# Kernel optimization log

Measured on AMD Instinct MI355X. Metric: run time of the kernel, lower is better.

## Reference

```python
import jax, jax.numpy as jnp
import numpy as np
from jax import lax

EPS = 1e-5

def setup_inputs() -> dict:
    key = jax.random.key(0)
    k1, k2 = jax.random.split(key)
    x = jax.random.normal(k1, (8, 256, 64, 64), dtype=jnp.float32)
    W = jax.random.normal(k2, (128, 256, 5, 5), dtype=jnp.float32) * 0.02
    gamma = jnp.ones((128,), dtype=jnp.float32)
    beta = jnp.zeros((128,), dtype=jnp.float32)
    return {"x": x, "W": W, "gamma": gamma, "beta": beta}

def reference(x, W, gamma, beta):
    B, C, H, Wd = x.shape
    # bilinear x2 upsample, half-pixel centers (== torch align_corners=False)
    up = jax.image.resize(x, (B, C, 2 * H, 2 * Wd), method="bilinear")
    # conv2d, stride 1, padding 2, no bias (norm == 'BN')
    out = lax.conv_general_dilated(
        up, W, window_strides=(1, 1), padding=[(2, 2), (2, 2)],
        dimension_numbers=("NCHW", "OIHW", "NCHW"))
    # BatchNorm2d (batch statistics, training-style refresh)
    mean = jnp.mean(out, axis=(0, 2, 3))
    var = jnp.var(out, axis=(0, 2, 3))
    inv = gamma / jnp.sqrt(var + EPS)
    out = (out - mean[None, :, None, None]) * inv[None, :, None, None] + beta[None, :, None, None]
    # activation: torch.relu
    return jax.nn.relu(out)
```

## Files before the change

kernel.cpp:

```cpp
#include <hip/hip_runtime.h>
#include <hip/hip_bf16.h>
#include <stdint.h>

typedef short s8v __attribute__((ext_vector_type(8)));
typedef float f4v __attribute__((ext_vector_type(4)));

__device__ __forceinline__ void async_copy16(const void* gsrc, void* lds_dst) {
  __builtin_amdgcn_global_load_lds(
      (const __attribute__((address_space(1))) uint32_t*)(uintptr_t)gsrc,
      (__attribute__((address_space(3))) uint32_t*)(uint32_t)(uintptr_t)lds_dst,
      16, 0, 0);
}

#define WAITVM(N) asm volatile("s_waitcnt vmcnt(" #N ")" ::: "memory")
__device__ __forceinline__ void block_barrier() {
  asm volatile("" ::: "memory");
  __builtin_amdgcn_s_barrier();
  asm volatile("" ::: "memory");
}

__global__ __launch_bounds__(256) void wpack_kernel(const float* __restrict__ W,
                                                    __hip_bfloat16* __restrict__ Wr,
                                                    float* __restrict__ gstats) {
  __shared__ __hip_bfloat16 t[256 * 26];
  const int co = blockIdx.x;
  const int tid = threadIdx.x;
  if (co == 0) gstats[tid] = 0.f;
  const float* src = W + co * 6400;
  for (int i = tid; i < 6400; i += 256) {
    int ci = i / 25;
    int pos = i - ci * 25;
    t[ci * 26 + pos] = __float2bfloat16(src[i]);
  }
  __syncthreads();
  for (int pos = 0; pos < 25; ++pos)
    Wr[pos * 32768 + co * 256 + tid] = t[tid * 26 + pos];
}

__global__ __launch_bounds__(256, 2) void upsample_kernel(const float* __restrict__ x,
                                                          __hip_bfloat16* __restrict__ up) {
  __shared__ __hip_bfloat16 lx[10 * 48 * 66];
  const int tid = threadIdx.x;
  const int bx = blockIdx.x;
  const int owb = bx & 1;
  const int ohb = (bx >> 1) & 7;
  const int cb = (bx >> 4) & 3;
  const int b = bx >> 6;
  const int oh0 = ohb * 16, ow0 = owb * 64, c0 = cb * 64;
  const int ih0 = (oh0 >> 1) - 1;
  const int iw_lo = (ow0 >> 1) - 1;
  const int aligned = (iw_lo < 0 ? 0 : iw_lo) & ~15;

  for (int i = tid; i < 64 * 10 * 12; i += 256) {
    int c = i / 120;
    int rem = i - c * 120;
    int r = rem / 12;
    int w4 = (rem - r * 12) * 4;
    int gr = ih0 + r;
    gr = gr < 0 ? 0 : (gr > 63 ? 63 : gr);
    const float4 v = *(const float4*)&x[(((b * 256 + c0 + c) * 64) + gr) * 64 + aligned + w4];
    int base = (r * 48 + w4) * 66 + c;
    lx[base]       = __float2bfloat16(v.x);
    lx[base + 66]  = __float2bfloat16(v.y);
    lx[base + 132] = __float2bfloat16(v.z);
    lx[base + 198] = __float2bfloat16(v.w);
  }
  __syncthreads();

  const int c2 = (tid & 31) * 2;
  const int owq = tid >> 5;
  uint32_t* upu = (uint32_t*)up;
  for (int it = 0; it < 128; ++it) {
    int oh_l = it >> 3;
    int ow_l = (it & 7) * 8 + owq;
    int oh = oh0 + oh_l, ow = ow0 + ow_l;
    int ihA = (oh >> 1) - ((oh & 1) ^ 1);
    float wh = (oh & 1) ? 0.75f : 0.25f;
    int iwA = (ow >> 1) - ((ow & 1) ^ 1);
    float wwt = (ow & 1) ? 0.75f : 0.25f;
    int r0 = ihA - ih0;
    int w0 = (iwA < 0 ? 0 : iwA) - aligned;
    int w1t = iwA + 1; w1t = w1t > 63 ? 63 : w1t;
    int w1 = w1t - aligned;
    uint32_t t00 = *(const uint32_t*)&lx[(r0 * 48 + w0) * 66 + c2];
    uint32_t t01 = *(const uint32_t*)&lx[(r0 * 48 + w1) * 66 + c2];
    uint32_t t10 = *(const uint32_t*)&lx[((r0 + 1) * 48 + w0) * 66 + c2];
    uint32_t t11 = *(const uint32_t*)&lx[((r0 + 1) * 48 + w1) * 66 + c2];
    float wlo = wh * wwt, wlo1 = wh * (1.f - wwt);
    float whi = (1.f - wh) * wwt, whi1 = (1.f - wh) * (1.f - wwt);
    float vlo = wlo * __uint_as_float(t00 << 16) + wlo1 * __uint_as_float(t01 << 16) +
                whi * __uint_as_float(t10 << 16) + whi1 * __uint_as_float(t11 << 16);
    float vhi = wlo * __uint_as_float(t00 & 0xffff0000u) + wlo1 * __uint_as_float(t01 & 0xffff0000u) +
                whi * __uint_as_float(t10 & 0xffff0000u) + whi1 * __uint_as_float(t11 & 0xffff0000u);
    __hip_bfloat16 h0 = __float2bfloat16(vlo);
    __hip_bfloat16 h1 = __float2bfloat16(vhi);
    uint32_t pk = (uint32_t)(*(unsigned short*)&h0) | ((uint32_t)(*(unsigned short*)&h1) << 16);
    upu[((((size_t)(b * 128 + oh) * 128) + ow) * 256 + c0 + c2) >> 1] = pk;
  }
}

#define ASLOT 8448
__global__ __launch_bounds__(512, 2) void conv_kernel(const __hip_bfloat16* __restrict__ up,
                                                      const __hip_bfloat16* __restrict__ Wr,
                                                      float* __restrict__ out,
                                                      float* __restrict__ gstats) {
  __shared__ __align__(16) unsigned short lA[5 * ASLOT];
  __shared__ __align__(16) unsigned short lB[3][128 * 64];
  __shared__ float lsum[128], lssq[128];

  const int tid = threadIdx.x;
  const int lane = tid & 63;
  const int wave = tid >> 6;
  const int wm = wave >> 1;
  const int wn = wave & 1;
  const int lane15 = lane & 15;
  const int quad = lane >> 4;
  const int wb = wave << 6;

  const int bid = blockIdx.x;
  const int orig = ((bid & 7) << 5) | (bid >> 3);
  const int b = orig >> 5;
  const int oh0 = (orig & 31) << 2;

  const f4v zero4 = {0.f, 0.f, 0.f, 0.f};
  if (tid < 128) { lsum[tid] = 0.f; lssq[tid] = 0.f; }
  if (tid < 160) {
    int s = tid >> 5, j = tid & 31;
    int rsel = j >> 3;
    int r = (rsel < 2) ? rsel : (128 + rsel);
    *(f4v*)&lA[s * ASLOT + (r * 8 + (j & 7)) * 8] = zero4;
  }

  auto stageA = [&](int slot, const __hip_bfloat16* uprow) {
#pragma unroll
    for (int t = 0; t < 2; ++t) {
      int pl = t * 512 + wb + lane;
      int riw = pl >> 3, pc = pl & 7;
      int r = riw + 2;
      int cq = pc ^ (r & 7);
      async_copy16(uprow + riw * 256 + cq * 8, (void*)&lA[slot * ASLOT + (16 + t * 512 + wb) * 8]);
    }
  };
  auto stageB = [&](const __hip_bfloat16* wsrc, int bsel) {
#pragma unroll
    for (int t = 0; t < 2; ++t) {
      int pl = t * 512 + wb + lane;
      int n = pl >> 3, pc = pl & 7;
      int cq = pc ^ (n & 7);
      async_copy16(wsrc + n * 256 + cq * 8, (void*)&lB[bsel][(t * 512 + wb) * 8]);
    }
  };

  f4v acc[8][4];
#pragma unroll
  for (int i = 0; i < 8; ++i)
#pragma unroll
    for (int j = 0; j < 4; ++j) acc[i][j] = zero4;

  for (int rr = 0; rr < 4; ++rr) {
    int ih = oh0 + rr - 2;
    if ((unsigned)ih < 128u)
      stageA(ih % 5, up + (size_t)(b * 128 + ih) * 32768);
  }
  stageB(Wr, 0);
  __syncthreads();

  int bcur = 0;
  for (int cb = 0; cb < 4; ++cb) {
    const int c0 = cb << 6;
    for (int kh = 0; kh < 5; ++kh) {
      const int ih = oh0 + wm + kh - 2;
      const bool rowok = (unsigned)ih < 128u;
      const int abase = rowok ? (ih % 5) * ASLOT : 0;
      for (int kw = 0; kw < 5; ++kw) {
        const int pos = kh * 5 + kw;
        const int bnext = (bcur == 2) ? 0 : bcur + 1;
        if (cb != 0 && kh == 0 && kw == 0) {
          for (int rr = 0; rr < 4; ++rr) {
            int ihn = oh0 + rr - 2;
            if ((unsigned)ihn < 128u)
              stageA(ihn % 5, up + (size_t)(b * 128 + ihn) * 32768 + c0);
          }
        }
        if (pos < 24)      stageB(Wr + (size_t)(pos + 1) * 32768 + c0, bnext);
        else if (cb < 3)   stageB(Wr + (c0 + 64), bnext);
        const bool extraA = (kw == 2) && (kh < 4) && (oh0 + kh + 2 < 128);
        if (extraA)
          stageA((oh0 + kh + 2) % 5, up + (size_t)(b * 128 + oh0 + kh + 2) * 32768 + c0);
        if (pos == 24 && cb == 3) { WAITVM(0); }
        else if (extraA)          { WAITVM(4); }
        else                      { WAITVM(2); }
        block_barrier();
        if (rowok) {
          __builtin_amdgcn_s_setprio(1);
#pragma unroll
          for (int ks = 0; ks < 2; ++ks) {
            const int cq = ks * 4 + quad;
            s8v a[8], bb[4];
#pragma unroll
            for (int mt = 0; mt < 8; ++mt) {
              int r = mt * 16 + lane15 + kw;
              a[mt] = *(const s8v*)&lA[abase + (r * 8 + (cq ^ (r & 7))) * 8];
            }
#pragma unroll
            for (int nt = 0; nt < 4; ++nt) {
              int n = (wn << 6) + nt * 16 + lane15;
              bb[nt] = *(const s8v*)&lB[bcur][(n * 8 + (cq ^ (n & 7))) * 8];
            }
#pragma unroll
            for (int mt = 0; mt < 8; ++mt)
#pragma unroll
              for (int nt = 0; nt < 4; ++nt)
                acc[mt][nt] = __builtin_amdgcn_mfma_f32_16x16x32_bf16(a[mt], bb[nt], acc[mt][nt], 0, 0, 0);
          }
          __builtin_amdgcn_s_setprio(0);
        }
        if (pos == 24 && cb < 3) block_barrier();
        bcur = bnext;
      }
    }
  }

  const int oh = oh0 + wm;
#pragma unroll
  for (int nt = 0; nt < 4; ++nt) {
    const int n = (wn << 6) + nt * 16 + lane15;
    float* oc = out + ((size_t)(b * 128 + n) * 128 + oh) * 128;
    float s = 0.f, ss = 0.f;
#pragma unroll
    for (int mt = 0; mt < 8; ++mt) {
      f4v v = acc[mt][nt];
      *(f4v*)&oc[mt * 16 + (quad << 2)] = v;
      s += v.x + v.y + v.z + v.w;
      ss += v.x * v.x + v.y * v.y + v.z * v.z + v.w * v.w;
    }
    s += __shfl_xor(s, 16, 64); ss += __shfl_xor(ss, 16, 64);
    s += __shfl_xor(s, 32, 64); ss += __shfl_xor(ss, 32, 64);
    if (quad == 0) { atomicAdd(&lsum[n], s); atomicAdd(&lssq[n], ss); }
  }
  __syncthreads();
  if (tid < 128) {
    atomicAdd(&gstats[tid], lsum[tid]);
    atomicAdd(&gstats[128 + tid], lssq[tid]);
  }
}

__global__ __launch_bounds__(256) void norm_kernel(float* __restrict__ out,
                                                   const float* __restrict__ gstats,
                                                   const float* __restrict__ gamma,
                                                   const float* __restrict__ beta) {
  for (int i = blockIdx.x * 256 + threadIdx.x; i < 4194304; i += 2048 * 256) {
    f4v v = ((f4v*)out)[i];
    int c = (i >> 12) & 127;
    float mean = gstats[c] * (1.f / 131072.f);
    float var = gstats[128 + c] * (1.f / 131072.f) - mean * mean;
    float sc = gamma[c] * rsqrtf(var + 1e-5f);
    float bi = beta[c] - mean * sc;
    v.x = fmaxf(fmaf(v.x, sc, bi), 0.f);
    v.y = fmaxf(fmaf(v.y, sc, bi), 0.f);
    v.z = fmaxf(fmaf(v.z, sc, bi), 0.f);
    v.w = fmaxf(fmaf(v.w, sc, bi), 0.f);
    ((f4v*)out)[i] = v;
  }
}

extern "C" void kernel_launch(void* const* d_in, const int* in_sizes, int n_in,
                              void* d_out, int out_size, void* d_ws, size_t ws_size,
                              hipStream_t stream) {
  (void)in_sizes; (void)n_in; (void)out_size; (void)ws_size;
  const float* x = (const float*)d_in[0];
  const float* W = (const float*)d_in[1];
  const float* gamma = (const float*)d_in[2];
  const float* beta = (const float*)d_in[3];
  float* out = (float*)d_out;
  char* ws = (char*)d_ws;
  __hip_bfloat16* up = (__hip_bfloat16*)ws;
  __hip_bfloat16* Wr = (__hip_bfloat16*)(ws + 67108864);
  float* gstats = (float*)(ws + 67108864 + 1638400);

  wpack_kernel<<<128, 256, 0, stream>>>(W, Wr, gstats);
  upsample_kernel<<<512, 256, 0, stream>>>(x, up);
  conv_kernel<<<256, 512, 0, stream>>>(up, Wr, out, gstats);
  norm_kernel<<<2048, 256, 0, stream>>>(out, gstats, gamma, beta);
}
```

Baseline: 297.2 us.

## Split conv tiles along width to double grid and halve per-block accumulators

The conv kernel now covers half the output width per block (64 columns plus halo), so the grid doubles to 512 blocks. Each wave holds half as many accumulators, and the A slot and B ring buffers shrink so four blocks can fit per CU. Out-of-range halo columns are loaded from a zero global buffer instead of pre-zeroed LDS. The B buffer drops from triple to double buffering, which adds a barrier every step and halves the MFMA work done per weight-tile load.

```diff
diff --git a/kernel.cpp b/kernel.cpp
--- a/kernel.cpp
+++ b/kernel.cpp
@@ -4,6 +4,8 @@
 
 typedef short s8v __attribute__((ext_vector_type(8)));
 typedef float f4v __attribute__((ext_vector_type(4)));
+
+__device__ __align__(16) float g_zeros[4] = {0.f, 0.f, 0.f, 0.f};
 
 __device__ __forceinline__ void async_copy16(const void* gsrc, void* lds_dst) {
   __builtin_amdgcn_global_load_lds(
@@ -99,13 +101,13 @@
   }
 }
 
-#define ASLOT 8448
-__global__ __launch_bounds__(512, 2) void conv_kernel(const __hip_bfloat16* __restrict__ up,
+#define ASLOT 4608
+__global__ __launch_bounds__(512, 4) void conv_kernel(const __hip_bfloat16* __restrict__ up,
                                                       const __hip_bfloat16* __restrict__ Wr,
                                                       float* __restrict__ out,
                                                       float* __restrict__ gstats) {
   __shared__ __align__(16) unsigned short lA[5 * ASLOT];
-  __shared__ __align__(16) unsigned short lB[3][128 * 64];
+  __shared__ __align__(16) unsigned short lB[2][128 * 64];
   __shared__ float lsum[128], lssq[128];
 
   const int tid = threadIdx.x;
@@ -118,27 +120,30 @@
   const int wb = wave << 6;
 
   const int bid = blockIdx.x;
-  const int orig = ((bid & 7) << 5) | (bid >> 3);
-  const int b = orig >> 5;
-  const int oh0 = (orig & 31) << 2;
+  const int orig = ((bid & 7) << 6) | (bid >> 3);
+  const int b = orig >> 6;
+  const int oh0 = ((orig >> 1) & 31) << 2;
+  const int ow0 = (orig & 1) << 6;
 
   const f4v zero4 = {0.f, 0.f, 0.f, 0.f};
   if (tid < 128) { lsum[tid] = 0.f; lssq[tid] = 0.f; }
-  if (tid < 160) {
-    int s = tid >> 5, j = tid & 31;
-    int rsel = j >> 3;
-    int r = (rsel < 2) ? rsel : (128 + rsel);
-    *(f4v*)&lA[s * ASLOT + (r * 8 + (j & 7)) * 8] = zero4;
-  }
 
   auto stageA = [&](int slot, const __hip_bfloat16* uprow) {
-#pragma unroll
-    for (int t = 0; t < 2; ++t) {
-      int pl = t * 512 + wb + lane;
-      int riw = pl >> 3, pc = pl & 7;
-      int r = riw + 2;
-      int cq = pc ^ (r & 7);
-      async_copy16(uprow + riw * 256 + cq * 8, (void*)&lA[slot * ASLOT + (16 + t * 512 + wb) * 8]);
+    int idx = wb + lane;
+    int r = idx >> 3, pc = idx & 7;
+    int cq = pc ^ (r & 7);
+    int iw = ow0 - 4 + r;
+    const void* src = ((unsigned)iw < 128u) ? (const void*)(uprow + iw * 256 + cq * 8)
+                                            : (const void*)g_zeros;
+    async_copy16(src, (void*)&lA[(slot * 576 + wb) * 8]);
+    if (wave == 0) {
+      int idx2 = 512 + lane;
+      int r2 = idx2 >> 3, pc2 = idx2 & 7;
+      int cq2 = pc2 ^ (r2 & 7);
+      int iw2 = ow0 - 4 + r2;
+      const void* src2 = ((unsigned)iw2 < 128u) ? (const void*)(uprow + iw2 * 256 + cq2 * 8)
+                                                : (const void*)g_zeros;
+      async_copy16(src2, (void*)&lA[(slot * 576 + 512) * 8]);
     }
   };
   auto stageB = [&](const __hip_bfloat16* wsrc, int bsel) {
@@ -151,9 +156,9 @@
     }
   };
 
-  f4v acc[8][4];
-#pragma unroll
-  for (int i = 0; i < 8; ++i)
+  f4v acc[4][4];
+#pragma unroll
+  for (int i = 0; i < 4; ++i)
 #pragma unroll
     for (int j = 0; j < 4; ++j) acc[i][j] = zero4;
 
@@ -165,7 +170,7 @@
   stageB(Wr, 0);
   __syncthreads();
 
-  int bcur = 0;
+  int buf = 0;
   for (int cb = 0; cb < 4; ++cb) {
     const int c0 = cb << 6;
     for (int kh = 0; kh < 5; ++kh) {
@@ -174,49 +179,49 @@
       const int abase = rowok ? (ih % 5) * ASLOT : 0;
       for (int kw = 0; kw < 5; ++kw) {
         const int pos = kh * 5 + kw;
-        const int bnext = (bcur == 2) ? 0 : bcur + 1;
-        if (cb != 0 && kh == 0 && kw == 0) {
+        if (cb != 0 && pos == 0) {
           for (int rr = 0; rr < 4; ++rr) {
             int ihn = oh0 + rr - 2;
             if ((unsigned)ihn < 128u)
               stageA(ihn % 5, up + (size_t)(b * 128 + ihn) * 32768 + c0);
           }
         }
-        if (pos < 24)      stageB(Wr + (size_t)(pos + 1) * 32768 + c0, bnext);
-        else if (cb < 3)   stageB(Wr + (c0 + 64), bnext);
+        if (pos < 24)      stageB(Wr + (size_t)(pos + 1) * 32768 + c0, buf ^ 1);
+        else if (cb < 3)   stageB(Wr + (c0 + 64), buf ^ 1);
         const bool extraA = (kw == 2) && (kh < 4) && (oh0 + kh + 2 < 128);
         if (extraA)
           stageA((oh0 + kh + 2) % 5, up + (size_t)(b * 128 + oh0 + kh + 2) * 32768 + c0);
-        if (pos == 24 && cb == 3) { WAITVM(0); }
-        else if (extraA)          { WAITVM(4); }
-        else                      { WAITVM(2); }
+        if (pos == 24 && cb == 3)      { WAITVM(0); }
+        else if (cb != 0 && pos == 0)  { WAITVM(6); }
+        else if (extraA)               { WAITVM(3); }
+        else                           { WAITVM(2); }
         block_barrier();
         if (rowok) {
           __builtin_amdgcn_s_setprio(1);
 #pragma unroll
           for (int ks = 0; ks < 2; ++ks) {
             const int cq = ks * 4 + quad;
-            s8v a[8], bb[4];
-#pragma unroll
-            for (int mt = 0; mt < 8; ++mt) {
-              int r = mt * 16 + lane15 + kw;
+            s8v a[4], bb[4];
+#pragma unroll
+            for (int mt = 0; mt < 4; ++mt) {
+              int r = mt * 16 + lane15 + kw + 2;
               a[mt] = *(const s8v*)&lA[abase + (r * 8 + (cq ^ (r & 7))) * 8];
             }
 #pragma unroll
             for (int nt = 0; nt < 4; ++nt) {
               int n = (wn << 6) + nt * 16 + lane15;
-              bb[nt] = *(const s8v*)&lB[bcur][(n * 8 + (cq ^ (n & 7))) * 8];
+              bb[nt] = *(const s8v*)&lB[buf][(n * 8 + (cq ^ (n & 7))) * 8];
             }
 #pragma unroll
-            for (int mt = 0; mt < 8; ++mt)
+            for (int mt = 0; mt < 4; ++mt)
 #pragma unroll
               for (int nt = 0; nt < 4; ++nt)
                 acc[mt][nt] = __builtin_amdgcn_mfma_f32_16x16x32_bf16(a[mt], bb[nt], acc[mt][nt], 0, 0, 0);
           }
           __builtin_amdgcn_s_setprio(0);
         }
-        if (pos == 24 && cb < 3) block_barrier();
-        bcur = bnext;
+        block_barrier();
+        buf ^= 1;
       }
     }
   }
@@ -225,10 +230,10 @@
 #pragma unroll
   for (int nt = 0; nt < 4; ++nt) {
     const int n = (wn << 6) + nt * 16 + lane15;
-    float* oc = out + ((size_t)(b * 128 + n) * 128 + oh) * 128;
+    float* oc = out + ((size_t)(b * 128 + n) * 128 + oh) * 128 + ow0;
     float s = 0.f, ss = 0.f;
 #pragma unroll
-    for (int mt = 0; mt < 8; ++mt) {
+    for (int mt = 0; mt < 4; ++mt) {
       f4v v = acc[mt][nt];
       *(f4v*)&oc[mt * 16 + (quad << 2)] = v;
       s += v.x + v.y + v.z + v.w;
@@ -280,6 +285,6 @@
 
   wpack_kernel<<<128, 256, 0, stream>>>(W, Wr, gstats);
   upsample_kernel<<<512, 256, 0, stream>>>(x, up);
-  conv_kernel<<<256, 512, 0, stream>>>(up, Wr, out, gstats);
+  conv_kernel<<<512, 512, 0, stream>>>(up, Wr, out, gstats);
   norm_kernel<<<2048, 256, 0, stream>>>(out, gstats, gamma, beta);
 }
```

Result: slower. 340.8 us (+14.7%).

## Software-pipeline LDS fragment loads with MFMA and deepen weight ring buffer

Applied to the files above, without the earlier changes.

Flattens the cb/kh/kw loops into one loop over 100 steps and double-buffers the register fragments, so the ks=0 operands for the next step are read from LDS while the current ks=1 MFMAs run. The weight staging ring grows from 3 to 4 buffers with a prefetch distance of two steps, so the next weight tile is already resident when it is read early. The cost is more LDS (an extra 16 KB), which may strain 2-blocks-per-CU occupancy, plus extra fragment registers. The wait counts must also stay correct for the new prefetch distance.

```diff
diff --git a/kernel.cpp b/kernel.cpp
--- a/kernel.cpp
+++ b/kernel.cpp
@@ -100,12 +100,39 @@
 }
 
 #define ASLOT 8448
+
+#define READ_A(S, KH, KW, KS)                                                 \
+  { int ihr_ = oh0 + wm + (KH) - 2;                                           \
+    if ((unsigned)ihr_ < 128u) {                                              \
+      const unsigned short* ap_ = &lA[(ihr_ % 5) * ASLOT];                    \
+      const int cqa_ = (KS) * 4 + quad;                                       \
+      _Pragma("unroll") for (int mt = 0; mt < 8; ++mt) {                      \
+        int r_ = mt * 16 + lane15 + (KW);                                     \
+        fa##S[mt] = *(const s8v*)&ap_[(r_ * 8 + (cqa_ ^ (r_ & 7))) * 8];      \
+      } } }
+
+#define READ_B(S, BUF, KS)                                                    \
+  { const unsigned short* bp_ = lB[BUF];                                      \
+    const int cqb_ = (KS) * 4 + quad;                                         \
+    _Pragma("unroll") for (int nt = 0; nt < 4; ++nt) {                        \
+      int n_ = (wn << 6) + nt * 16 + lane15;                                  \
+      fb##S[nt] = *(const s8v*)&bp_[(n_ * 8 + (cqb_ ^ (n_ & 7))) * 8];        \
+    } }
+
+#define DO_MFMA(S)                                                            \
+  if (rowok_) {                                                               \
+    _Pragma("unroll") for (int mt = 0; mt < 8; ++mt)                          \
+      _Pragma("unroll") for (int nt = 0; nt < 4; ++nt)                        \
+        acc[mt][nt] = __builtin_amdgcn_mfma_f32_16x16x32_bf16(                \
+            fa##S[mt], fb##S[nt], acc[mt][nt], 0, 0, 0);                      \
+  }
+
 __global__ __launch_bounds__(512, 2) void conv_kernel(const __hip_bfloat16* __restrict__ up,
                                                       const __hip_bfloat16* __restrict__ Wr,
                                                       float* __restrict__ out,
                                                       float* __restrict__ gstats) {
   __shared__ __align__(16) unsigned short lA[5 * ASLOT];
-  __shared__ __align__(16) unsigned short lB[3][128 * 64];
+  __shared__ __align__(16) unsigned short lB[4][128 * 64];
   __shared__ float lsum[128], lssq[128];
 
   const int tid = threadIdx.x;
@@ -157,68 +184,64 @@
 #pragma unroll
     for (int j = 0; j < 4; ++j) acc[i][j] = zero4;
 
+  s8v fa0[8], fb0[4];
+  s8v fa1[8], fb1[4];
+
   for (int rr = 0; rr < 4; ++rr) {
     int ih = oh0 + rr - 2;
     if ((unsigned)ih < 128u)
       stageA(ih % 5, up + (size_t)(b * 128 + ih) * 32768);
   }
   stageB(Wr, 0);
+  stageB(Wr + 32768, 1);
   __syncthreads();
 
-  int bcur = 0;
-  for (int cb = 0; cb < 4; ++cb) {
-    const int c0 = cb << 6;
-    for (int kh = 0; kh < 5; ++kh) {
-      const int ih = oh0 + wm + kh - 2;
-      const bool rowok = (unsigned)ih < 128u;
-      const int abase = rowok ? (ih % 5) * ASLOT : 0;
-      for (int kw = 0; kw < 5; ++kw) {
-        const int pos = kh * 5 + kw;
-        const int bnext = (bcur == 2) ? 0 : bcur + 1;
-        if (cb != 0 && kh == 0 && kw == 0) {
-          for (int rr = 0; rr < 4; ++rr) {
-            int ihn = oh0 + rr - 2;
-            if ((unsigned)ihn < 128u)
-              stageA(ihn % 5, up + (size_t)(b * 128 + ihn) * 32768 + c0);
-          }
-        }
-        if (pos < 24)      stageB(Wr + (size_t)(pos + 1) * 32768 + c0, bnext);
-        else if (cb < 3)   stageB(Wr + (c0 + 64), bnext);
-        const bool extraA = (kw == 2) && (kh < 4) && (oh0 + kh + 2 < 128);
-        if (extraA)
-          stageA((oh0 + kh + 2) % 5, up + (size_t)(b * 128 + oh0 + kh + 2) * 32768 + c0);
-        if (pos == 24 && cb == 3) { WAITVM(0); }
-        else if (extraA)          { WAITVM(4); }
-        else                      { WAITVM(2); }
-        block_barrier();
-        if (rowok) {
-          __builtin_amdgcn_s_setprio(1);
-#pragma unroll
-          for (int ks = 0; ks < 2; ++ks) {
-            const int cq = ks * 4 + quad;
-            s8v a[8], bb[4];
-#pragma unroll
-            for (int mt = 0; mt < 8; ++mt) {
-              int r = mt * 16 + lane15 + kw;
-              a[mt] = *(const s8v*)&lA[abase + (r * 8 + (cq ^ (r & 7))) * 8];
-            }
-#pragma unroll
-            for (int nt = 0; nt < 4; ++nt) {
-              int n = (wn << 6) + nt * 16 + lane15;
-              bb[nt] = *(const s8v*)&lB[bcur][(n * 8 + (cq ^ (n & 7))) * 8];
-            }
-#pragma unroll
-            for (int mt = 0; mt < 8; ++mt)
-#pragma unroll
-              for (int nt = 0; nt < 4; ++nt)
-                acc[mt][nt] = __builtin_amdgcn_mfma_f32_16x16x32_bf16(a[mt], bb[nt], acc[mt][nt], 0, 0, 0);
-          }
-          __builtin_amdgcn_s_setprio(0);
-        }
-        if (pos == 24 && cb < 3) block_barrier();
-        bcur = bnext;
+  READ_A(0, 0, 0, 0);
+  READ_B(0, 0, 0);
+
+#pragma unroll 1
+  for (int t_ = 0; t_ < 100; ++t_) {
+    const int cb_ = t_ / 25, pos_ = t_ % 25;
+    const int kh_ = pos_ / 5, kw_ = pos_ % 5;
+    const int c0_ = cb_ << 6;
+    const bool bnd_ = (cb_ != 0 && pos_ == 0);
+    if (bnd_) {
+      for (int rr_ = 0; rr_ < 4; ++rr_) {
+        int ihn_ = oh0 + rr_ - 2;
+        if ((unsigned)ihn_ < 128u)
+          stageA(ihn_ % 5, up + (size_t)(b * 128 + ihn_) * 32768 + c0_);
       }
     }
+    if (t_ <= 97) {
+      const int tt_ = t_ + 2;
+      stageB(Wr + (size_t)(tt_ % 25) * 32768 + ((tt_ / 25) << 6), tt_ & 3);
+    }
+    const bool exA_ = (kw_ == 2) && (kh_ < 4) && (oh0 + kh_ + 2 < 128);
+    if (exA_)
+      stageA((oh0 + kh_ + 2) % 5, up + (size_t)(b * 128 + oh0 + kh_ + 2) * 32768 + c0_);
+    if (t_ > 97)      { WAITVM(0); }
+    else if (bnd_)    { WAITVM(2); }
+    else if (exA_)    { WAITVM(4); }
+    else              { WAITVM(2); }
+    block_barrier();
+    const int ih_ = oh0 + wm + kh_ - 2;
+    const bool rowok_ = (unsigned)ih_ < 128u;
+    __builtin_amdgcn_s_setprio(1);
+    if (bnd_) {
+      READ_A(0, kh_, kw_, 0);
+      READ_B(0, t_ & 3, 0);
+    }
+    READ_A(1, kh_, kw_, 1);
+    READ_B(1, t_ & 3, 1);
+    DO_MFMA(0);
+    if (t_ < 99 && ((t_ + 1) % 25) != 0) {
+      const int p1_ = (t_ + 1) % 25;
+      READ_A(0, p1_ / 5, p1_ % 5, 0);
+      READ_B(0, (t_ + 1) & 3, 0);
+    }
+    DO_MFMA(1);
+    __builtin_amdgcn_s_setprio(0);
+    if (pos_ == 24 && cb_ < 3) block_barrier();
   }
 
   const int oh = oh0 + wm;
```

New measurement: 332.7 us. 11.9% more time.

## Fuse weight pack, upsample, conv and batchnorm into one persistent kernel

Applied to the files above, without the earlier changes.

Merges the four launches into a single 256-block kernel that packs the weights, builds the upsampled bf16 tile, then synchronises the grid with an atomic-counter barrier before the MFMA convolution. A second grid barrier after the statistics reduction lets each block apply batchnorm and ReLU directly to its register accumulators. This removes the fp32 output round trip through global memory and the separate norm pass, plus launch overhead. The cost is two spin-wait grid barriers that assume all 256 blocks are co-resident, and an upsample phase that now runs on fewer, larger blocks.

```diff
diff --git a/kernel.cpp b/kernel.cpp
--- a/kernel.cpp
+++ b/kernel.cpp
@@ -19,91 +19,29 @@
   asm volatile("" ::: "memory");
 }
 
-__global__ __launch_bounds__(256) void wpack_kernel(const float* __restrict__ W,
-                                                    __hip_bfloat16* __restrict__ Wr,
-                                                    float* __restrict__ gstats) {
-  __shared__ __hip_bfloat16 t[256 * 26];
-  const int co = blockIdx.x;
-  const int tid = threadIdx.x;
-  if (co == 0) gstats[tid] = 0.f;
-  const float* src = W + co * 6400;
-  for (int i = tid; i < 6400; i += 256) {
-    int ci = i / 25;
-    int pos = i - ci * 25;
-    t[ci * 26 + pos] = __float2bfloat16(src[i]);
-  }
-  __syncthreads();
-  for (int pos = 0; pos < 25; ++pos)
-    Wr[pos * 32768 + co * 256 + tid] = t[tid * 26 + pos];
-}
-
-__global__ __launch_bounds__(256, 2) void upsample_kernel(const float* __restrict__ x,
-                                                          __hip_bfloat16* __restrict__ up) {
-  __shared__ __hip_bfloat16 lx[10 * 48 * 66];
-  const int tid = threadIdx.x;
-  const int bx = blockIdx.x;
-  const int owb = bx & 1;
-  const int ohb = (bx >> 1) & 7;
-  const int cb = (bx >> 4) & 3;
-  const int b = bx >> 6;
-  const int oh0 = ohb * 16, ow0 = owb * 64, c0 = cb * 64;
-  const int ih0 = (oh0 >> 1) - 1;
-  const int iw_lo = (ow0 >> 1) - 1;
-  const int aligned = (iw_lo < 0 ? 0 : iw_lo) & ~15;
-
-  for (int i = tid; i < 64 * 10 * 12; i += 256) {
-    int c = i / 120;
-    int rem = i - c * 120;
-    int r = rem / 12;
-    int w4 = (rem - r * 12) * 4;
-    int gr = ih0 + r;
-    gr = gr < 0 ? 0 : (gr > 63 ? 63 : gr);
-    const float4 v = *(const float4*)&x[(((b * 256 + c0 + c) * 64) + gr) * 64 + aligned + w4];
-    int base = (r * 48 + w4) * 66 + c;
-    lx[base]       = __float2bfloat16(v.x);
-    lx[base + 66]  = __float2bfloat16(v.y);
-    lx[base + 132] = __float2bfloat16(v.z);
-    lx[base + 198] = __float2bfloat16(v.w);
-  }
-  __syncthreads();
-
-  const int c2 = (tid & 31) * 2;
-  const int owq = tid >> 5;
-  uint32_t* upu = (uint32_t*)up;
-  for (int it = 0; it < 128; ++it) {
-    int oh_l = it >> 3;
-    int ow_l = (it & 7) * 8 + owq;
-    int oh = oh0 + oh_l, ow = ow0 + ow_l;
-    int ihA = (oh >> 1) - ((oh & 1) ^ 1);
-    float wh = (oh & 1) ? 0.75f : 0.25f;
-    int iwA = (ow >> 1) - ((ow & 1) ^ 1);
-    float wwt = (ow & 1) ? 0.75f : 0.25f;
-    int r0 = ihA - ih0;
-    int w0 = (iwA < 0 ? 0 : iwA) - aligned;
-    int w1t = iwA + 1; w1t = w1t > 63 ? 63 : w1t;
-    int w1 = w1t - aligned;
-    uint32_t t00 = *(const uint32_t*)&lx[(r0 * 48 + w0) * 66 + c2];
-    uint32_t t01 = *(const uint32_t*)&lx[(r0 * 48 + w1) * 66 + c2];
-    uint32_t t10 = *(const uint32_t*)&lx[((r0 + 1) * 48 + w0) * 66 + c2];
-    uint32_t t11 = *(const uint32_t*)&lx[((r0 + 1) * 48 + w1) * 66 + c2];
-    float wlo = wh * wwt, wlo1 = wh * (1.f - wwt);
-    float whi = (1.f - wh) * wwt, whi1 = (1.f - wh) * (1.f - wwt);
-    float vlo = wlo * __uint_as_float(t00 << 16) + wlo1 * __uint_as_float(t01 << 16) +
-                whi * __uint_as_float(t10 << 16) + whi1 * __uint_as_float(t11 << 16);
-    float vhi = wlo * __uint_as_float(t00 & 0xffff0000u) + wlo1 * __uint_as_float(t01 & 0xffff0000u) +
-                whi * __uint_as_float(t10 & 0xffff0000u) + whi1 * __uint_as_float(t11 & 0xffff0000u);
-    __hip_bfloat16 h0 = __float2bfloat16(vlo);
-    __hip_bfloat16 h1 = __float2bfloat16(vhi);
-    uint32_t pk = (uint32_t)(*(unsigned short*)&h0) | ((uint32_t)(*(unsigned short*)&h1) << 16);
-    upu[((((size_t)(b * 128 + oh) * 128) + ow) * 256 + c0 + c2) >> 1] = pk;
-  }
+__device__ __forceinline__ void grid_barrier(int* ctr) {
+  __threadfence();
+  __syncthreads();
+  if (threadIdx.x == 0) {
+    atomicAdd(ctr, 1);
+    while (__hip_atomic_load(ctr, __ATOMIC_ACQUIRE, __HIP_MEMORY_SCOPE_AGENT) < 256) {
+      __builtin_amdgcn_s_sleep(8);
+    }
+  }
+  __syncthreads();
+  __threadfence();
 }
 
 #define ASLOT 8448
-__global__ __launch_bounds__(512, 2) void conv_kernel(const __hip_bfloat16* __restrict__ up,
-                                                      const __hip_bfloat16* __restrict__ Wr,
-                                                      float* __restrict__ out,
-                                                      float* __restrict__ gstats) {
+__global__ __launch_bounds__(512, 2) void fused_kernel(const float* __restrict__ x,
+                                                       const float* __restrict__ W,
+                                                       __hip_bfloat16* __restrict__ up,
+                                                       __hip_bfloat16* __restrict__ Wr,
+                                                       float* __restrict__ out,
+                                                       float* __restrict__ gstats,
+                                                       const float* __restrict__ gamma,
+                                                       const float* __restrict__ beta,
+                                                       int* __restrict__ bar) {
   __shared__ __align__(16) unsigned short lA[5 * ASLOT];
   __shared__ __align__(16) unsigned short lB[3][128 * 64];
   __shared__ float lsum[128], lssq[128];
@@ -121,6 +59,76 @@
   const int orig = ((bid & 7) << 5) | (bid >> 3);
   const int b = orig >> 5;
   const int oh0 = (orig & 31) << 2;
+
+  if (bid < 128) {
+    __hip_bfloat16* tw = (__hip_bfloat16*)lB;
+    const float* src = W + bid * 6400;
+    for (int i = tid; i < 6400; i += 512) {
+      int ci = i / 25;
+      int pos = i - ci * 25;
+      tw[ci * 26 + pos] = __float2bfloat16(src[i]);
+    }
+    __syncthreads();
+    for (int j = tid; j < 25 * 256; j += 512) {
+      int pos = j >> 8, ci = j & 255;
+      Wr[pos * 32768 + bid * 256 + ci] = tw[ci * 26 + pos];
+    }
+  }
+
+  {
+    __hip_bfloat16* lx = (__hip_bfloat16*)lA;
+    const int ih0 = (oh0 >> 1) - 1;
+    const int c2 = (tid & 31) * 2;
+    const int owq = tid >> 5;
+    uint32_t* upu = (uint32_t*)up;
+    for (int cb = 0; cb < 4; ++cb) {
+      const int c0 = cb * 64;
+      __syncthreads();
+      for (int i = tid; i < 4096; i += 512) {
+        int c = i >> 6;
+        int rem = i & 63;
+        int r = rem >> 4;
+        int w4 = (rem & 15) * 4;
+        int gr = ih0 + r;
+        gr = gr < 0 ? 0 : (gr > 63 ? 63 : gr);
+        const float4 v = *(const float4*)&x[(((b * 256 + c0 + c) * 64) + gr) * 64 + w4];
+        int base = (r * 64 + w4) * 66 + c;
+        lx[base]       = __float2bfloat16(v.x);
+        lx[base + 66]  = __float2bfloat16(v.y);
+        lx[base + 132] = __float2bfloat16(v.z);
+        lx[base + 198] = __float2bfloat16(v.w);
+      }
+      __syncthreads();
+      for (int it = 0; it < 32; ++it) {
+        int oh_l = it >> 3;
+        int ow = (it & 7) * 16 + owq;
+        int oh = oh0 + oh_l;
+        int ihA = (oh >> 1) - ((oh & 1) ^ 1);
+        float wh = (oh & 1) ? 0.75f : 0.25f;
+        int iwA = (ow >> 1) - ((ow & 1) ^ 1);
+        float wwt = (ow & 1) ? 0.75f : 0.25f;
+        int r0 = ihA - ih0;
+        int w0 = iwA < 0 ? 0 : iwA;
+        int w1 = iwA + 1; w1 = w1 > 63 ? 63 : w1;
+        uint32_t t00 = *(const uint32_t*)&lx[(r0 * 64 + w0) * 66 + c2];
+        uint32_t t01 = *(const uint32_t*)&lx[(r0 * 64 + w1) * 66 + c2];
+        uint32_t t10 = *(const uint32_t*)&lx[((r0 + 1) * 64 + w0) * 66 + c2];
+        uint32_t t11 = *(const uint32_t*)&lx[((r0 + 1) * 64 + w1) * 66 + c2];
+        float wlo = wh * wwt, wlo1 = wh * (1.f - wwt);
+        float whi = (1.f - wh) * wwt, whi1 = (1.f - wh) * (1.f - wwt);
+        float vlo = wlo * __uint_as_float(t00 << 16) + wlo1 * __uint_as_float(t01 << 16) +
+                    whi * __uint_as_float(t10 << 16) + whi1 * __uint_as_float(t11 << 16);
+        float vhi = wlo * __uint_as_float(t00 & 0xffff0000u) + wlo1 * __uint_as_float(t01 & 0xffff0000u) +
+                    whi * __uint_as_float(t10 & 0xffff0000u) + whi1 * __uint_as_float(t11 & 0xffff0000u);
+        __hip_bfloat16 h0 = __float2bfloat16(vlo);
+        __hip_bfloat16 h1 = __float2bfloat16(vhi);
+        uint32_t pk = (uint32_t)(*(unsigned short*)&h0) | ((uint32_t)(*(unsigned short*)&h1) << 16);
+        upu[((((size_t)(b * 128 + oh) * 128) + ow) * 256 + c0 + c2) >> 1] = pk;
+      }
+    }
+  }
+
+  grid_barrier(bar);
 
   const f4v zero4 = {0.f, 0.f, 0.f, 0.f};
   if (tid < 128) { lsum[tid] = 0.f; lssq[tid] = 0.f; }
@@ -221,16 +229,13 @@
     }
   }
 
-  const int oh = oh0 + wm;
 #pragma unroll
   for (int nt = 0; nt < 4; ++nt) {
     const int n = (wn << 6) + nt * 16 + lane15;
-    float* oc = out + ((size_t)(b * 128 + n) * 128 + oh) * 128;
     float s = 0.f, ss = 0.f;
 #pragma unroll
     for (int mt = 0; mt < 8; ++mt) {
       f4v v = acc[mt][nt];
-      *(f4v*)&oc[mt * 16 + (quad << 2)] = v;
       s += v.x + v.y + v.z + v.w;
       ss += v.x * v.x + v.y * v.y + v.z * v.z + v.w * v.w;
     }
@@ -243,24 +248,27 @@
     atomicAdd(&gstats[tid], lsum[tid]);
     atomicAdd(&gstats[128 + tid], lssq[tid]);
   }
-}
-
-__global__ __launch_bounds__(256) void norm_kernel(float* __restrict__ out,
-                                                   const float* __restrict__ gstats,
-                                                   const float* __restrict__ gamma,
-                                                   const float* __restrict__ beta) {
-  for (int i = blockIdx.x * 256 + threadIdx.x; i < 4194304; i += 2048 * 256) {
-    f4v v = ((f4v*)out)[i];
-    int c = (i >> 12) & 127;
-    float mean = gstats[c] * (1.f / 131072.f);
-    float var = gstats[128 + c] * (1.f / 131072.f) - mean * mean;
-    float sc = gamma[c] * rsqrtf(var + 1e-5f);
-    float bi = beta[c] - mean * sc;
-    v.x = fmaxf(fmaf(v.x, sc, bi), 0.f);
-    v.y = fmaxf(fmaf(v.y, sc, bi), 0.f);
-    v.z = fmaxf(fmaf(v.z, sc, bi), 0.f);
-    v.w = fmaxf(fmaf(v.w, sc, bi), 0.f);
-    ((f4v*)out)[i] = v;
+
+  grid_barrier(bar + 1);
+
+  const int oh = oh0 + wm;
+#pragma unroll
+  for (int nt = 0; nt < 4; ++nt) {
+    const int n = (wn << 6) + nt * 16 + lane15;
+    float mean = gstats[n] * (1.f / 131072.f);
+    float var = gstats[128 + n] * (1.f / 131072.f) - mean * mean;
+    float sc = gamma[n] * rsqrtf(var + 1e-5f);
+    float bi = beta[n] - mean * sc;
+    float* oc = out + ((size_t)(b * 128 + n) * 128 + oh) * 128;
+#pragma unroll
+    for (int mt = 0; mt < 8; ++mt) {
+      f4v v = acc[mt][nt];
+      v.x = fmaxf(fmaf(v.x, sc, bi), 0.f);
+      v.y = fmaxf(fmaf(v.y, sc, bi), 0.f);
+      v.z = fmaxf(fmaf(v.z, sc, bi), 0.f);
+      v.w = fmaxf(fmaf(v.w, sc, bi), 0.f);
+      *(f4v*)&oc[mt * 16 + (quad << 2)] = v;
+    }
   }
 }
 
@@ -277,9 +285,8 @@
   __hip_bfloat16* up = (__hip_bfloat16*)ws;
   __hip_bfloat16* Wr = (__hip_bfloat16*)(ws + 67108864);
   float* gstats = (float*)(ws + 67108864 + 1638400);
-
-  wpack_kernel<<<128, 256, 0, stream>>>(W, Wr, gstats);
-  upsample_kernel<<<512, 256, 0, stream>>>(x, up);
-  conv_kernel<<<256, 512, 0, stream>>>(up, Wr, out, gstats);
-  norm_kernel<<<2048, 256, 0, stream>>>(out, gstats, gamma, beta);
-}
+  int* bar = (int*)(gstats + 256);
+
+  hipMemsetAsync(gstats, 0, 256 * sizeof(float) + 2 * sizeof(int), stream);
+  fused_kernel<<<256, 512, 0, stream>>>(x, W, up, Wr, out, gstats, gamma, beta, bar);
+}
```

After: 451.9 us. 1.52x slower.
